# Optimization experiments

Measured on AMD Instinct MI355X. Metric: run time of the kernel, lower is better.

The kernel has to match this reference:

```python
import jax, jax.numpy as jnp
import numpy as np

N_NODES = 100000
N_EDGES = 400000
IN_DIM = 100
OUT_DIM = 200
NUM_STEPS = 4


def setup_inputs() -> dict:
    key = jax.random.key(0)
    ks = jax.random.split(key, 8)
    x = jax.random.normal(ks[0], (N_NODES, IN_DIM), dtype=jnp.float32)
    edge_index = jax.random.randint(ks[1], (2, N_EDGES), 0, N_NODES, dtype=jnp.int64)
    s = 0.05
    W = jax.random.normal(ks[2], (NUM_STEPS, OUT_DIM, OUT_DIM), dtype=jnp.float32) * s
    w_ih = jax.random.normal(ks[3], (3 * OUT_DIM, OUT_DIM), dtype=jnp.float32) * s
    w_hh = jax.random.normal(ks[4], (3 * OUT_DIM, OUT_DIM), dtype=jnp.float32) * s
    b_ih = jax.random.normal(ks[5], (3 * OUT_DIM,), dtype=jnp.float32) * s
    b_hh = jax.random.normal(ks[6], (3 * OUT_DIM,), dtype=jnp.float32) * s
    cls_w = jax.random.normal(ks[7], (2, OUT_DIM), dtype=jnp.float32) * s
    cls_b = jnp.zeros((2,), dtype=jnp.float32)
    return {"x": x, "W": W, "w_ih": w_ih, "w_hh": w_hh, "b_ih": b_ih,
            "b_hh": b_hh, "cls_w": cls_w, "cls_b": cls_b, "edge_index": edge_index}


def _gru_cell(a, h, w_ih, w_hh, b_ih, b_hh):
    # torch.nn.GRUCell math: input a, hidden h
    gi = a @ w_ih.T + b_ih          # [N, 3D]
    gh = h @ w_hh.T + b_hh          # [N, 3D]
    i_r, i_z, i_n = jnp.split(gi, 3, axis=1)
    h_r, h_z, h_n = jnp.split(gh, 3, axis=1)
    r = jax.nn.sigmoid(i_r + h_r)
    z = jax.nn.sigmoid(i_z + h_z)
    n = jnp.tanh(i_n + r * h_n)
    return (1.0 - z) * n + z * h


def reference(x, W, w_ih, w_hh, b_ih, b_hh, cls_w, cls_b, edge_index):
    N = x.shape[0]
    # GatedGraphConv pads input features with zeros up to out_channels
    h = jnp.pad(x, ((0, 0), (0, OUT_DIM - x.shape[1])))
    src, dst = edge_index[0], edge_index[1]
    for i in range(NUM_STEPS):
        m = h @ W[i]                                         # [N, D]
        aggr = jax.ops.segment_sum(m[src], dst, num_segments=N)  # scatter-add
        h = _gru_cell(aggr, h, w_ih, w_hh, b_ih, b_hh)
    out = jax.nn.relu(h)
    # global_max_pool with all-zero batch ids -> max over all nodes
    pooled = jnp.max(out, axis=0, keepdims=True)             # [1, D]
    logits = pooled @ cls_w.T + cls_b                        # [1, 2]
    return jax.nn.softmax(logits, axis=1)
```

## Files before the change

### kernel.cpp

```cpp
#include <hip/hip_runtime.h>
#include <hip/hip_bf16.h>
#include <math.h>

#define N_NODES 100000
#define N_PAD   100096
#define N_EDGES 400000
#define IN_DIM  100
#define D       200
#define DP      208
#define KP      224
#define NUM_STEPS 4

#define TILE_SHORTS  21504
#define HALF_SHORTS  10752
#define HALF_GROUPS  21
#define EIDX_CAP     896

typedef __attribute__((ext_vector_type(8))) short bfrag;
typedef __attribute__((ext_vector_type(4))) float facc;

__device__ float g_Wc[NUM_STEPS * 600 * D];
__device__ short g_Wall[NUM_STEPS * 13 * TILE_SHORTS];
__device__ float g_bias[6 * DP];

__device__ __forceinline__ float fast_sigmoid(float x) {
    return __builtin_amdgcn_rcpf(1.0f + __expf(-x));
}
__device__ __forceinline__ float fast_tanh(float x) {
    return 2.0f * __builtin_amdgcn_rcpf(1.0f + __expf(-2.0f * x)) - 1.0f;
}
__device__ __forceinline__ float bf2f(short u) {
    unsigned int x = ((unsigned int)(unsigned short)u) << 16;
    return __uint_as_float(x);
}

__global__ __launch_bounds__(256) void wc_kernel(const float* __restrict__ W,
                                                 const float* __restrict__ w_ih) {
    int s = blockIdx.x / 600;
    int j = blockIdx.x % 600;
    int k = threadIdx.x;
    if (k >= D) return;
    const float* wr = &w_ih[(size_t)j * D];
    const float* Wr = &W[(size_t)s * D * D + (size_t)k * D];
    float acc = 0.0f;
    #pragma unroll 4
    for (int t = 0; t < D; ++t) acc += wr[t] * Wr[t];
    g_Wc[((size_t)s * 600 + j) * D + k] = acc;
}

__global__ __launch_bounds__(256) void wconv_kernel(const float* __restrict__ w_hh) {
    int idx = blockIdx.x * 256 + threadIdx.x;
    int l  = idx & 63;
    int t  = (idx >> 6) % 7;
    int g  = (idx / 448) % 6;
    int jt = (idx / 2688) % 13;
    int s  = idx / 34944;
    int j  = jt * 16 + (l & 15);
    int k0 = t * 32 + (l >> 4) * 8;
    short* out = g_Wall + (size_t)idx * 8;
    #pragma unroll
    for (int i = 0; i < 8; ++i) {
        int k = k0 + i;
        float v = 0.0f;
        if (j < D && k < D)
            v = (g < 3) ? g_Wc[((size_t)s * 600 + g * 200 + j) * D + k]
                        : w_hh[((size_t)(g - 3) * 200 + j) * D + k];
        __hip_bfloat16 b = __float2bfloat16(v);
        out[i] = *reinterpret_cast<short*>(&b);
    }
}

__global__ void bias_kernel(const float* __restrict__ b_ih, const float* __restrict__ b_hh) {
    int idx = blockIdx.x * 256 + threadIdx.x;
    if (idx >= 6 * DP) return;
    int g = idx / DP, j = idx % DP;
    float v = 0.0f;
    if (j < D) v = (g < 3) ? b_ih[g * 200 + j] : b_hh[(g - 3) * 200 + j];
    g_bias[idx] = v;
}

__global__ void pad_kernel(const float* __restrict__ x, __hip_bfloat16* __restrict__ h) {
    int idx = blockIdx.x * 256 + threadIdx.x;
    int n = idx / KP, c = idx % KP;
    float v = (n < N_NODES && c < IN_DIM) ? x[n * IN_DIM + c] : 0.0f;
    h[idx] = __float2bfloat16(v);
}

__global__ void count_kernel(const int* __restrict__ dst, int* __restrict__ cnt) {
    int e = blockIdx.x * blockDim.x + threadIdx.x;
    if (e < N_EDGES) atomicAdd(&cnt[dst[e]], 1);
}

#define SCAN_B 1024
__global__ __launch_bounds__(SCAN_B) void scan1(const int* __restrict__ cnt,
                                                int* __restrict__ incl, int* __restrict__ bsum) {
    __shared__ int ws[16];
    int i = blockIdx.x * SCAN_B + threadIdx.x;
    int lane = threadIdx.x & 63, wid = threadIdx.x >> 6;
    int v = (i < N_NODES) ? cnt[i] : 0;
    int s = v;
    #pragma unroll
    for (int o = 1; o < 64; o <<= 1) {
        int t = __shfl_up(s, o, 64);
        if (lane >= o) s += t;
    }
    if (lane == 63) ws[wid] = s;
    __syncthreads();
    if (wid == 0) {
        int t = (lane < 16) ? ws[lane] : 0;
        #pragma unroll
        for (int o = 1; o < 16; o <<= 1) {
            int u = __shfl_up(t, o, 64);
            if (lane >= o) t += u;
        }
        if (lane < 16) ws[lane] = t;
    }
    __syncthreads();
    if (wid > 0) s += ws[wid - 1];
    if (i < N_NODES) incl[i] = s;
    if (threadIdx.x == SCAN_B - 1) bsum[blockIdx.x] = s;
}
__global__ void scan2(int* __restrict__ bsum, int nb) {
    __shared__ int sh[128];
    int v = (threadIdx.x < nb) ? bsum[threadIdx.x] : 0;
    sh[threadIdx.x] = v; __syncthreads();
    for (int off = 1; off < 128; off <<= 1) {
        int t = (threadIdx.x >= off) ? sh[threadIdx.x - off] : 0;
        __syncthreads();
        sh[threadIdx.x] += t;
        __syncthreads();
    }
    if (threadIdx.x < nb) bsum[threadIdx.x] = sh[threadIdx.x] - v;
}
__global__ void scan3(const int* __restrict__ cnt, const int* __restrict__ incl,
                      const int* __restrict__ bsum, int* __restrict__ off,
                      int* __restrict__ cursor) {
    int i = blockIdx.x * blockDim.x + threadIdx.x;
    if (i < N_NODES) {
        int v = incl[i] - cnt[i] + bsum[i / SCAN_B];
        off[i] = v; cursor[i] = v;
    }
    if (i == 0) off[N_NODES] = N_EDGES;
}
__global__ void fill_kernel(const int* __restrict__ src, const int* __restrict__ dst,
                            int* __restrict__ cursor, int* __restrict__ esrc) {
    int e = blockIdx.x * blockDim.x + threadIdx.x;
    if (e < N_EDGES) {
        int pos = atomicAdd(&cursor[dst[e]], 1);
        esrc[pos] = src[e];
    }
}

__device__ __forceinline__ void stage_half(const short* __restrict__ gsrc,
                                           short* lds_dst, int wave, int lane) {
    #pragma unroll
    for (int g = wave; g < HALF_GROUPS; g += 4) {
        __builtin_amdgcn_global_load_lds(
            (const __attribute__((address_space(1))) void*)(gsrc + g * 512 + lane * 8),
            (__attribute__((address_space(3))) void*)(lds_dst + g * 512),
            16, 0, 0);
    }
}

__global__ __launch_bounds__(256, 2) void gru_fused(const __hip_bfloat16* __restrict__ hcur,
                                                    __hip_bfloat16* __restrict__ hnext,
                                                    const int* __restrict__ off,
                                                    const int* __restrict__ esrc,
                                                    unsigned int* __restrict__ pooled,
                                                    int step) {
    __shared__ short Bs[2][HALF_SHORTS];
    __shared__ unsigned int pmax[DP];
    int tid = threadIdx.x;
    int lane = tid & 63, wave = tid >> 6;
    int wbase = blockIdx.x * 128 + wave * 32;
    int mrow = lane & 15, kq = lane >> 4;
    bool dopool = (step == NUM_STEPS - 1);

    if (dopool) for (int c = tid; c < DP; c += 256) pmax[c] = 0u;

    short* LDSbase = &Bs[0][0];
    short* Awave = LDSbase + wave * 16 * KP;
    int* EIdx = (int*)((char*)LDSbase + 28672) + wave * EIDX_CAP;

    int nlo = wbase < N_NODES ? wbase : N_NODES;
    int nhi = (wbase + 32) < N_NODES ? (wbase + 32) : N_NODES;
    int lo = off[nlo];
    int cntw = off[nhi] - lo;
    bool use_lds = (cntw <= EIDX_CAP);
    if (use_lds)
        for (int i = lane; i < cntw; i += 64) EIdx[i] = esrc[lo + i];

    bfrag av[2][7], hv[2][7];

    int r4 = lane >> 4;
    int ck = lane & 15;
    int colA = ck * 8;
    int colB = colA + 128;
    bool sumB = (ck < 9);
    #pragma unroll
    for (int p = 0; p < 2; ++p) {
        #pragma unroll
        for (int it = 0; it < 4; ++it) {
            int rr = it * 4 + r4;
            int n = wbase + p * 16 + rr;
            float a[8] = {0, 0, 0, 0, 0, 0, 0, 0};
            float b[8] = {0, 0, 0, 0, 0, 0, 0, 0};
            if (n < N_NODES) {
                int e0 = off[n] - lo, e1 = off[n + 1] - lo;
                int e = e0;
                for (; e + 3 < e1; e += 4) {
                    int i0, i1, i2, i3;
                    if (use_lds) {
                        i0 = EIdx[e]; i1 = EIdx[e + 1]; i2 = EIdx[e + 2]; i3 = EIdx[e + 3];
                    } else {
                        i0 = esrc[lo + e];     i1 = esrc[lo + e + 1];
                        i2 = esrc[lo + e + 2]; i3 = esrc[lo + e + 3];
                    }
                    size_t s0 = (size_t)i0 * KP, s1 = (size_t)i1 * KP;
                    size_t s2 = (size_t)i2 * KP, s3 = (size_t)i3 * KP;
                    bfrag a0 = *(const bfrag*)(hcur + s0 + colA);
                    bfrag a1 = *(const bfrag*)(hcur + s1 + colA);
                    bfrag a2 = *(const bfrag*)(hcur + s2 + colA);
                    bfrag a3 = *(const bfrag*)(hcur + s3 + colA);
                    if (sumB) {
                        bfrag b0 = *(const bfrag*)(hcur + s0 + colB);
                        bfrag b1 = *(const bfrag*)(hcur + s1 + colB);
                        bfrag b2 = *(const bfrag*)(hcur + s2 + colB);
                        bfrag b3 = *(const bfrag*)(hcur + s3 + colB);
                        #pragma unroll
                        for (int q = 0; q < 8; ++q)
                            b[q] += (bf2f(b0[q]) + bf2f(b1[q])) + (bf2f(b2[q]) + bf2f(b3[q]));
                    }
                    #pragma unroll
                    for (int q = 0; q < 8; ++q)
                        a[q] += (bf2f(a0[q]) + bf2f(a1[q])) + (bf2f(a2[q]) + bf2f(a3[q]));
                }
                for (; e < e1; ++e) {
                    int i0 = use_lds ? EIdx[e] : esrc[lo + e];
                    size_t s0 = (size_t)i0 * KP;
                    bfrag a0 = *(const bfrag*)(hcur + s0 + colA);
                    if (sumB) {
                        bfrag b0 = *(const bfrag*)(hcur + s0 + colB);
                        #pragma unroll
                        for (int q = 0; q < 8; ++q) b[q] += bf2f(b0[q]);
                    }
                    #pragma unroll
                    for (int q = 0; q < 8; ++q) a[q] += bf2f(a0[q]);
                }
            }
            __hip_bfloat16 oa[8], ob[8];
            #pragma unroll
            for (int q = 0; q < 8; ++q) {
                oa[q] = __float2bfloat16(a[q]);
                ob[q] = __float2bfloat16(b[q]);
            }
            *(ushort4*)(Awave + rr * KP + colA)     = *(const ushort4*)&oa[0];
            *(ushort4*)(Awave + rr * KP + colA + 4) = *(const ushort4*)&oa[4];
            if (ck < 12) {
                *(ushort4*)(Awave + rr * KP + colB)     = *(const ushort4*)&ob[0];
                *(ushort4*)(Awave + rr * KP + colB + 4) = *(const ushort4*)&ob[4];
            }
        }
        #pragma unroll
        for (int t = 0; t < 7; ++t)
            av[p][t] = *(const bfrag*)&Awave[mrow * KP + t * 32 + kq * 8];
    }

    size_t hbase = (size_t)(wbase + mrow) * KP + kq * 8;
    #pragma unroll
    for (int mf = 0; mf < 2; ++mf)
        #pragma unroll
        for (int t = 0; t < 7; ++t)
            hv[mf][t] = *(const bfrag*)(hcur + hbase + mf * 16 * KP + t * 32);

    const short* Wstep = g_Wall + (size_t)step * 13 * TILE_SHORTS;
    int jcol = lane & 15;
    int rowq = (lane >> 4) * 4;

    __syncthreads();
    stage_half(Wstep, &Bs[0][0], wave, lane);

    facc acc[6][2];
    unsigned short hold_u[2][4];

    for (int hk = 0; hk < 26; ++hk) {
        __syncthreads();
        if (hk + 1 < 26)
            stage_half(Wstep + (size_t)(hk + 1) * HALF_SHORTS,
                       &Bs[(hk + 1) & 1][0], wave, lane);

        int jt = hk >> 1;
        int j = jt * 16 + jcol;
        const short* Bcur = &Bs[hk & 1][0];

        if ((hk & 1) == 0) {
            #pragma unroll
            for (int mf = 0; mf < 2; ++mf)
                #pragma unroll
                for (int r = 0; r < 4; ++r)
                    hold_u[mf][r] = *(const unsigned short*)
                        (hcur + (size_t)(wbase + mf * 16 + rowq + r) * KP + j);
            #pragma unroll
            for (int g = 0; g < 6; ++g)
                #pragma unroll
                for (int mf = 0; mf < 2; ++mf) acc[g][mf] = (facc)(0.0f);
            #pragma unroll
            for (int t = 0; t < 7; ++t) {
                bfrag bv[3];
                #pragma unroll
                for (int g = 0; g < 3; ++g)
                    bv[g] = *(const bfrag*)&Bcur[(size_t)(((g * 7 + t) * 64) + lane) * 8];
                #pragma unroll
                for (int g = 0; g < 3; ++g)
                    #pragma unroll
                    for (int mf = 0; mf < 2; ++mf)
                        acc[g][mf] = __builtin_amdgcn_mfma_f32_16x16x32_bf16(av[mf][t], bv[g], acc[g][mf], 0, 0, 0);
            }
        } else {
            #pragma unroll
            for (int t = 0; t < 7; ++t) {
                bfrag bv[3];
                #pragma unroll
                for (int g = 0; g < 3; ++g)
                    bv[g] = *(const bfrag*)&Bcur[(size_t)(((g * 7 + t) * 64) + lane) * 8];
                #pragma unroll
                for (int g = 0; g < 3; ++g)
                    #pragma unroll
                    for (int mf = 0; mf < 2; ++mf)
                        acc[g + 3][mf] = __builtin_amdgcn_mfma_f32_16x16x32_bf16(hv[mf][t], bv[g], acc[g + 3][mf], 0, 0, 0);
            }

            float tmax = 0.0f;
            if (j < D) {
                float bir = g_bias[j],          biz = g_bias[DP + j],     bin = g_bias[2 * DP + j];
                float bhr = g_bias[3 * DP + j], bhz = g_bias[4 * DP + j], bhn = g_bias[5 * DP + j];
                #pragma unroll
                for (int mf = 0; mf < 2; ++mf) {
                    int m0 = wbase + mf * 16 + rowq;
                    #pragma unroll
                    for (int r = 0; r < 4; ++r) {
                        int m = m0 + r;
                        if (m < N_NODES) {
                            float hold = bf2f((short)hold_u[mf][r]);
                            float rr = fast_sigmoid(acc[0][mf][r] + bir + acc[3][mf][r] + bhr);
                            float zz = fast_sigmoid(acc[1][mf][r] + biz + acc[4][mf][r] + bhz);
                            float nn = fast_tanh(acc[2][mf][r] + bin + rr * (acc[5][mf][r] + bhn));
                            float hv2 = (1.0f - zz) * nn + zz * hold;
                            hnext[(size_t)m * KP + j] = __float2bfloat16(hv2);
                            if (hv2 > tmax) tmax = hv2;
                        }
                    }
                }
                if (dopool) atomicMax(&pmax[j], __float_as_uint(tmax));
            }
        }
    }

    if (dopool) {
        __syncthreads();
        for (int c = tid; c < D; c += 256) atomicMax(&pooled[c], pmax[c]);
    }
}

__global__ void head_kernel(const unsigned int* __restrict__ pooled,
                            const float* __restrict__ cls_w,
                            const float* __restrict__ cls_b,
                            float* __restrict__ out) {
    if (threadIdx.x == 0) {
        float l0 = cls_b[0], l1 = cls_b[1];
        for (int d = 0; d < D; ++d) {
            float p = __uint_as_float(pooled[d]);
            l0 += p * cls_w[d];
            l1 += p * cls_w[D + d];
        }
        float mx = l0 > l1 ? l0 : l1;
        float e0 = expf(l0 - mx), e1 = expf(l1 - mx);
        out[0] = e0 / (e0 + e1);
        out[1] = e1 / (e0 + e1);
    }
}

extern "C" void kernel_launch(void* const* d_in, const int* in_sizes, int n_in,
                              void* d_out, int out_size, void* d_ws, size_t ws_size,
                              hipStream_t stream) {
    const float* x     = (const float*)d_in[0];
    const float* W     = (const float*)d_in[1];
    const float* w_ih  = (const float*)d_in[2];
    const float* w_hh  = (const float*)d_in[3];
    const float* b_ih  = (const float*)d_in[4];
    const float* b_hh  = (const float*)d_in[5];
    const float* cls_w = (const float*)d_in[6];
    const float* cls_b = (const float*)d_in[7];
    const int*   ei    = (const int*)d_in[8];
    const int* src = ei;
    const int* dst = ei + N_EDGES;

    const size_t ROWB = (size_t)N_PAD * KP;
    __hip_bfloat16* hA   = (__hip_bfloat16*)d_ws;
    __hip_bfloat16* hB   = hA + ROWB;
    int* cnt    = (int*)(hB + ROWB);
    int* incl   = cnt + N_NODES;
    int* bsum   = incl + N_NODES;
    int* off    = bsum + 128;
    int* cursor = off + N_NODES + 1;
    int* esrc   = cursor + N_NODES;
    unsigned int* pooled = (unsigned int*)(esrc + N_EDGES);

    hipMemsetAsync(cnt, 0, N_NODES * sizeof(int), stream);
    count_kernel<<<(N_EDGES + 255) / 256, 256, 0, stream>>>(dst, cnt);
    scan1<<<(N_NODES + SCAN_B - 1) / SCAN_B, SCAN_B, 0, stream>>>(cnt, incl, bsum);
    scan2<<<1, 128, 0, stream>>>(bsum, (N_NODES + SCAN_B - 1) / SCAN_B);
    scan3<<<(N_NODES + 255) / 256, 256, 0, stream>>>(cnt, incl, bsum, off, cursor);
    fill_kernel<<<(N_EDGES + 255) / 256, 256, 0, stream>>>(src, dst, cursor, esrc);

    wc_kernel<<<NUM_STEPS * 600, 256, 0, stream>>>(W, w_ih);
    wconv_kernel<<<(NUM_STEPS * 13 * 6 * 7 * 64) / 256, 256, 0, stream>>>(w_hh);
    bias_kernel<<<(6 * DP + 255) / 256, 256, 0, stream>>>(b_ih, b_hh);

    pad_kernel<<<(int)(ROWB / 256), 256, 0, stream>>>(x, hA);
    hipMemsetAsync(pooled, 0, D * sizeof(unsigned int), stream);

    __hip_bfloat16* hcur = hA;
    __hip_bfloat16* hnext = hB;
    for (int s = 0; s < NUM_STEPS; ++s) {
        gru_fused<<<N_PAD / 128, 256, 0, stream>>>(hcur, hnext, off, esrc, pooled, s);
        __hip_bfloat16* t = hcur; hcur = hnext; hnext = t;
    }
    head_kernel<<<1, 64, 0, stream>>>(pooled, cls_w, cls_b, (float*)d_out);
}
```

Measured before the change: 841.6 us.

## Stage weights in thirds to cut LDS and raise GRU kernel occupancy

Splits each 16-column weight tile into three LDS stages of two gate groups each instead of two stages of three, shrinking the double buffer. The edge index cache gets its own smaller shared array, and launch bounds rise from 2 to 4 blocks per SM to allow more waves for latency hiding. The bias setup kernel is also folded into the weight conversion kernel to save a launch. The cost is more barriers per tile, a tighter register budget that may spill, and more wave groups falling back to global edge loads once they exceed the smaller index cache.

```diff
diff --git a/kernel.cpp b/kernel.cpp
--- a/kernel.cpp
+++ b/kernel.cpp
@@ -12,9 +12,9 @@
 #define NUM_STEPS 4
 
 #define TILE_SHORTS  21504
-#define HALF_SHORTS  10752
-#define HALF_GROUPS  21
-#define EIDX_CAP     896
+#define STAGE_SHORTS 7168
+#define STAGE_GROUPS 14
+#define EIDX_CAP     512
 
 typedef __attribute__((ext_vector_type(8))) short bfrag;
 typedef __attribute__((ext_vector_type(4))) float facc;
@@ -48,7 +48,19 @@
     g_Wc[((size_t)s * 600 + j) * D + k] = acc;
 }
 
-__global__ __launch_bounds__(256) void wconv_kernel(const float* __restrict__ w_hh) {
+__global__ __launch_bounds__(256) void wconv_kernel(const float* __restrict__ w_hh,
+                                                    const float* __restrict__ b_ih,
+                                                    const float* __restrict__ b_hh) {
+    if (blockIdx.x >= 546) {
+        int idx = (blockIdx.x - 546) * 256 + threadIdx.x;
+        if (idx < 6 * DP) {
+            int g = idx / DP, j = idx % DP;
+            float v = 0.0f;
+            if (j < D) v = (g < 3) ? b_ih[g * 200 + j] : b_hh[(g - 3) * 200 + j];
+            g_bias[idx] = v;
+        }
+        return;
+    }
     int idx = blockIdx.x * 256 + threadIdx.x;
     int l  = idx & 63;
     int t  = (idx >> 6) % 7;
@@ -70,15 +82,6 @@
     }
 }
 
-__global__ void bias_kernel(const float* __restrict__ b_ih, const float* __restrict__ b_hh) {
-    int idx = blockIdx.x * 256 + threadIdx.x;
-    if (idx >= 6 * DP) return;
-    int g = idx / DP, j = idx % DP;
-    float v = 0.0f;
-    if (j < D) v = (g < 3) ? b_ih[g * 200 + j] : b_hh[(g - 3) * 200 + j];
-    g_bias[idx] = v;
-}
-
 __global__ void pad_kernel(const float* __restrict__ x, __hip_bfloat16* __restrict__ h) {
     int idx = blockIdx.x * 256 + threadIdx.x;
     int n = idx / KP, c = idx % KP;
@@ -151,10 +154,10 @@
     }
 }
 
-__device__ __forceinline__ void stage_half(const short* __restrict__ gsrc,
-                                           short* lds_dst, int wave, int lane) {
+__device__ __forceinline__ void stage_third(const short* __restrict__ gsrc,
+                                            short* lds_dst, int wave, int lane) {
     #pragma unroll
-    for (int g = wave; g < HALF_GROUPS; g += 4) {
+    for (int g = wave; g < STAGE_GROUPS; g += 4) {
         __builtin_amdgcn_global_load_lds(
             (const __attribute__((address_space(1))) void*)(gsrc + g * 512 + lane * 8),
             (__attribute__((address_space(3))) void*)(lds_dst + g * 512),
@@ -162,13 +165,14 @@
     }
 }
 
-__global__ __launch_bounds__(256, 2) void gru_fused(const __hip_bfloat16* __restrict__ hcur,
+__global__ __launch_bounds__(256, 4) void gru_fused(const __hip_bfloat16* __restrict__ hcur,
                                                     __hip_bfloat16* __restrict__ hnext,
                                                     const int* __restrict__ off,
                                                     const int* __restrict__ esrc,
                                                     unsigned int* __restrict__ pooled,
                                                     int step) {
-    __shared__ short Bs[2][HALF_SHORTS];
+    __shared__ short LDS[2 * STAGE_SHORTS];
+    __shared__ int eidx_s[4 * EIDX_CAP];
     __shared__ unsigned int pmax[DP];
     int tid = threadIdx.x;
     int lane = tid & 63, wave = tid >> 6;
@@ -178,9 +182,8 @@
 
     if (dopool) for (int c = tid; c < DP; c += 256) pmax[c] = 0u;
 
-    short* LDSbase = &Bs[0][0];
-    short* Awave = LDSbase + wave * 16 * KP;
-    int* EIdx = (int*)((char*)LDSbase + 28672) + wave * EIDX_CAP;
+    short* Awave = LDS + wave * 16 * KP;
+    int* EIdx = eidx_s + wave * EIDX_CAP;
 
     int nlo = wbase < N_NODES ? wbase : N_NODES;
     int nhi = (wbase + 32) < N_NODES ? (wbase + 32) : N_NODES;
@@ -278,22 +281,22 @@
     int rowq = (lane >> 4) * 4;
 
     __syncthreads();
-    stage_half(Wstep, &Bs[0][0], wave, lane);
+    stage_third(Wstep, &LDS[0], wave, lane);
 
     facc acc[6][2];
     unsigned short hold_u[2][4];
 
-    for (int hk = 0; hk < 26; ++hk) {
+    int jt = 0, ph = 0;
+    for (int ss = 0; ss < 39; ++ss) {
         __syncthreads();
-        if (hk + 1 < 26)
-            stage_half(Wstep + (size_t)(hk + 1) * HALF_SHORTS,
-                       &Bs[(hk + 1) & 1][0], wave, lane);
-
-        int jt = hk >> 1;
+        if (ss + 1 < 39)
+            stage_third(Wstep + (size_t)(ss + 1) * STAGE_SHORTS,
+                        &LDS[((ss + 1) & 1) * STAGE_SHORTS], wave, lane);
+
         int j = jt * 16 + jcol;
-        const short* Bcur = &Bs[hk & 1][0];
-
-        if ((hk & 1) == 0) {
+        const short* Bcur = &LDS[(ss & 1) * STAGE_SHORTS];
+
+        if (ph == 0) {
             #pragma unroll
             for (int mf = 0; mf < 2; ++mf)
                 #pragma unroll
@@ -306,28 +309,37 @@
                 for (int mf = 0; mf < 2; ++mf) acc[g][mf] = (facc)(0.0f);
             #pragma unroll
             for (int t = 0; t < 7; ++t) {
-                bfrag bv[3];
-                #pragma unroll
-                for (int g = 0; g < 3; ++g)
-                    bv[g] = *(const bfrag*)&Bcur[(size_t)(((g * 7 + t) * 64) + lane) * 8];
-                #pragma unroll
-                for (int g = 0; g < 3; ++g)
-                    #pragma unroll
-                    for (int mf = 0; mf < 2; ++mf)
-                        acc[g][mf] = __builtin_amdgcn_mfma_f32_16x16x32_bf16(av[mf][t], bv[g], acc[g][mf], 0, 0, 0);
-            }
+                bfrag bv0 = *(const bfrag*)&Bcur[(size_t)(((0 * 7 + t) * 64) + lane) * 8];
+                bfrag bv1 = *(const bfrag*)&Bcur[(size_t)(((1 * 7 + t) * 64) + lane) * 8];
+                #pragma unroll
+                for (int mf = 0; mf < 2; ++mf) {
+                    acc[0][mf] = __builtin_amdgcn_mfma_f32_16x16x32_bf16(av[mf][t], bv0, acc[0][mf], 0, 0, 0);
+                    acc[1][mf] = __builtin_amdgcn_mfma_f32_16x16x32_bf16(av[mf][t], bv1, acc[1][mf], 0, 0, 0);
+                }
+            }
+            ph = 1;
+        } else if (ph == 1) {
+            #pragma unroll
+            for (int t = 0; t < 7; ++t) {
+                bfrag bv0 = *(const bfrag*)&Bcur[(size_t)(((0 * 7 + t) * 64) + lane) * 8];
+                bfrag bv1 = *(const bfrag*)&Bcur[(size_t)(((1 * 7 + t) * 64) + lane) * 8];
+                #pragma unroll
+                for (int mf = 0; mf < 2; ++mf) {
+                    acc[2][mf] = __builtin_amdgcn_mfma_f32_16x16x32_bf16(av[mf][t], bv0, acc[2][mf], 0, 0, 0);
+                    acc[3][mf] = __builtin_amdgcn_mfma_f32_16x16x32_bf16(hv[mf][t], bv1, acc[3][mf], 0, 0, 0);
+                }
+            }
+            ph = 2;
         } else {
             #pragma unroll
             for (int t = 0; t < 7; ++t) {
-                bfrag bv[3];
-                #pragma unroll
-                for (int g = 0; g < 3; ++g)
-                    bv[g] = *(const bfrag*)&Bcur[(size_t)(((g * 7 + t) * 64) + lane) * 8];
-                #pragma unroll
-                for (int g = 0; g < 3; ++g)
-                    #pragma unroll
-                    for (int mf = 0; mf < 2; ++mf)
-                        acc[g + 3][mf] = __builtin_amdgcn_mfma_f32_16x16x32_bf16(hv[mf][t], bv[g], acc[g + 3][mf], 0, 0, 0);
+                bfrag bv0 = *(const bfrag*)&Bcur[(size_t)(((0 * 7 + t) * 64) + lane) * 8];
+                bfrag bv1 = *(const bfrag*)&Bcur[(size_t)(((1 * 7 + t) * 64) + lane) * 8];
+                #pragma unroll
+                for (int mf = 0; mf < 2; ++mf) {
+                    acc[4][mf] = __builtin_amdgcn_mfma_f32_16x16x32_bf16(hv[mf][t], bv0, acc[4][mf], 0, 0, 0);
+                    acc[5][mf] = __builtin_amdgcn_mfma_f32_16x16x32_bf16(hv[mf][t], bv1, acc[5][mf], 0, 0, 0);
+                }
             }
 
             float tmax = 0.0f;
@@ -353,6 +365,7 @@
                 }
                 if (dopool) atomicMax(&pmax[j], __float_as_uint(tmax));
             }
+            ph = 0; ++jt;
         }
     }
 
@@ -414,8 +427,7 @@
     fill_kernel<<<(N_EDGES + 255) / 256, 256, 0, stream>>>(src, dst, cursor, esrc);
 
     wc_kernel<<<NUM_STEPS * 600, 256, 0, stream>>>(W, w_ih);
-    wconv_kernel<<<(NUM_STEPS * 13 * 6 * 7 * 64) / 256, 256, 0, stream>>>(w_hh);
-    bias_kernel<<<(6 * DP + 255) / 256, 256, 0, stream>>>(b_ih, b_hh);
+    wconv_kernel<<<551, 256, 0, stream>>>(w_hh, b_ih, b_hh);
 
     pad_kernel<<<(int)(ROWB / 256), 256, 0, stream>>>(x, hA);
     hipMemsetAsync(pooled, 0, D * sizeof(unsigned int), stream);
```

Measured after the change: 1.922 ms. +128.4%, slower.
